# Kernel tuning notes

Measured on AMD Instinct MI355X. Metric: run time of the kernel, lower is better.

Reference implementation:

```python
import jax, jax.numpy as jnp
import numpy as np

N_NODES = 1_000_000
N_EDGES = 16_000_000
D = 30            # num_feature hardcoded in the module
WINDOW = D // 6   # = 5
DEG_THRESH = 10
NUM_TYPES = 2


def setup_inputs() -> dict:
    key = jax.random.key(0)
    k1, k2, k3, k4 = jax.random.split(key, 4)
    x = jax.random.normal(k1, (N_NODES, D), dtype=jnp.float32)
    W = jax.random.normal(k2, (D, D), dtype=jnp.float32)
    edge_index = jax.random.randint(k3, (2, N_EDGES), 0, N_NODES, dtype=jnp.int64)
    atom_types = jax.random.randint(k4, (N_NODES,), 0, NUM_TYPES, dtype=jnp.int64)
    return {"x": x, "W": W, "edge_index": edge_index, "atom_types": atom_types}


def reference(x, W, edge_index, atom_types):
    n = x.shape[0]
    # --- degree count: torch.bincount(edge_index.reshape(-1)) ---
    flat = edge_index.reshape(-1)
    count = jnp.zeros((n,), jnp.int32).at[flat].add(1)
    crit_count = (count > DEG_THRESH).astype(jnp.int32)  # criterion_count

    # --- type-mixture scatter-min over edges ---
    src, dst = edge_index[0], edge_index[1]
    same = atom_types[src] == atom_types[dst]
    # edge contributes 0 if types differ, else type+1, to BOTH endpoints; take min
    val = jnp.where(same, atom_types[src].astype(jnp.int32) + 1, 0)
    BIG = jnp.iinfo(jnp.int32).max
    mix = jnp.full((n,), BIG, jnp.int32)
    mix = mix.at[src].min(val).at[dst].min(val)
    mix = jnp.where(mix == BIG, 0, mix)  # isolated atoms -> 0

    crit = crit_count * 3 + mix  # criterion in [0, 5]

    # --- windowed one-hot criterion matrix [n, D] ---
    cols = jnp.arange(D, dtype=jnp.int32)
    start = (crit * WINDOW)[:, None]
    mask = ((cols[None, :] >= start) & (cols[None, :] < start + WINDOW)).astype(x.dtype)

    # --- e3nn Linear (30x0e -> 30x0e): dense matmul with 1/sqrt(fan_in) path norm ---
    scale = np.float32(1.0 / np.sqrt(D))
    return (x @ W) * scale * mask
```

## Files before the change

kernel.cpp:

```cpp
#include <hip/hip_runtime.h>

#define N_NODES    1000000
#define N_EDGES    16000000
#define D          30
#define WINDOW     5
#define DEG_THRESH 10

#define P_PARTS    31
#define PART_BITS  15
#define PART_SIZE  32768
#define CAP        1081344
#define BUF_CAP    512
#define BIN_BLOCKS 256
#define BIN_THREADS 1024
#define BIN_ITERS  16
#define N_GROUPS   (N_EDGES / 4)
#define BM_WORDS   (N_NODES / 32)

#define L_BM_BYTES   125000
#define L_BUF_BYTES  (P_PARTS * BUF_CAP * 2)
#define L_CNT_OFF    (L_BM_BYTES + L_BUF_BYTES)
#define L_TOTAL      (L_CNT_OFF + P_PARTS * 4 * 3)

#define SLICES     8
#define HIST_WORDS 16384

#define WS_BM_OFF      0
#define WS_CUR_OFF     131072
#define WS_PART_OFF    131328
#define WS_NEEDED      (WS_PART_OFF + (size_t)P_PARTS * SLICES * HIST_WORDS * 4)
#define OUT_BYTES_NEEDED ((size_t)P_PARTS * CAP * 2)

__global__ __launch_bounds__(256) void pack_types(
    const int* __restrict__ types,
    unsigned*  __restrict__ bm,
    unsigned*  __restrict__ cursors)
{
    const int g = blockIdx.x * 256 + threadIdx.x;
    const int v = (g < N_NODES) ? types[g] : 0;
    const unsigned long long m = __ballot(v);
    if ((threadIdx.x & 31) == 0 && g < N_NODES)
        bm[g >> 5] = (unsigned)(m >> (threadIdx.x & 32));
    if (blockIdx.x == 0 && threadIdx.x < 64) cursors[threadIdx.x] = 0u;
}

__global__ __launch_bounds__(BIN_THREADS, 1) void bin_edges(
    const int*      __restrict__ edge_index,
    const unsigned* __restrict__ bm,
    unsigned short* __restrict__ buckets,
    unsigned*       __restrict__ cursors)
{
    extern __shared__ char smem[];
    unsigned* bm_lds = (unsigned*)smem;
    unsigned short (*buf)[BUF_CAP] =
        (unsigned short(*)[BUF_CAP])(smem + L_BM_BYTES);
    unsigned* cnt   = (unsigned*)(smem + L_CNT_OFF);
    unsigned* basev = cnt + P_PARTS;
    unsigned* ccnt  = basev + P_PARTS;

    const int tid = threadIdx.x;
    for (int i = tid; i < BM_WORDS; i += BIN_THREADS) bm_lds[i] = bm[i];
    if (tid < P_PARTS) cnt[tid] = 0u;
    __syncthreads();

    for (int it = 0; it < BIN_ITERS; ++it) {
        const int g = (blockIdx.x * BIN_ITERS + it) * BIN_THREADS + tid;
        if (g < N_GROUPS) {
            const int e0 = g * 4;
            const int4 s4 = *reinterpret_cast<const int4*>(edge_index + e0);
            const int4 d4 = *reinterpret_cast<const int4*>(edge_index + N_EDGES + e0);
            const int ss[4] = {s4.x, s4.y, s4.z, s4.w};
            const int dd[4] = {d4.x, d4.y, d4.z, d4.w};
#pragma unroll
            for (int k = 0; k < 4; ++k) {
                const int s = ss[k], d = dd[k];
                const unsigned ts = (bm_lds[(unsigned)s >> 5] >> (s & 31)) & 1u;
                const unsigned td = (bm_lds[(unsigned)d >> 5] >> (d & 31)) & 1u;
                {
                    const int b = s >> PART_BITS;
                    const unsigned short rec =
                        (unsigned short)(((s & (PART_SIZE - 1)) << 1) | td);
                    const unsigned pos = atomicAdd(&cnt[b], 1u);
                    if (pos < BUF_CAP) buf[b][pos] = rec;
                    else {
                        const unsigned gp = atomicAdd(&cursors[b], 1u);
                        if (gp < CAP) buckets[(size_t)b * CAP + gp] = rec;
                    }
                }
                {
                    const int b = d >> PART_BITS;
                    const unsigned short rec =
                        (unsigned short)(((d & (PART_SIZE - 1)) << 1) | ts);
                    const unsigned pos = atomicAdd(&cnt[b], 1u);
                    if (pos < BUF_CAP) buf[b][pos] = rec;
                    else {
                        const unsigned gp = atomicAdd(&cursors[b], 1u);
                        if (gp < CAP) buckets[(size_t)b * CAP + gp] = rec;
                    }
                }
            }
        }
        __syncthreads();
        if (tid < P_PARTS) {
            unsigned c = cnt[tid]; if (c > BUF_CAP) c = BUF_CAP;
            unsigned bse = 0u;
            if (c) {
                bse = atomicAdd(&cursors[tid], c);
                if (bse > CAP) bse = CAP;
                if (bse + c > CAP) c = CAP - bse;
            }
            ccnt[tid] = c; basev[tid] = bse; cnt[tid] = 0u;
        }
        __syncthreads();
        const int w = tid >> 6, lane = tid & 63;
#pragma unroll
        for (int j = 0; j < 2; ++j) {
            const int b = w * 2 + j;
            if (b < P_PARTS) {
                const unsigned c = ccnt[b];
                unsigned short* dst = buckets + (size_t)b * CAP + basev[b];
                for (unsigned e = lane; e < c; e += 64) dst[e] = buf[b][e];
            }
        }
        __syncthreads();
    }
}

__global__ __launch_bounds__(512) void hist_pass(
    const unsigned short* __restrict__ buckets,
    const unsigned*       __restrict__ cursors,
    unsigned*             __restrict__ partials)
{
    __shared__ unsigned hist[HIST_WORDS];
    const int p = blockIdx.x >> 3, s = blockIdx.x & 7;
    const int tid = threadIdx.x;
    for (int i = tid; i < HIST_WORDS; i += 512) hist[i] = 0u;
    __syncthreads();

    unsigned count = cursors[p]; if (count > CAP) count = CAP;
    const unsigned short* bk = buckets + (size_t)p * CAP;
    const unsigned n4 = (count + 3u) >> 2;
    for (unsigned j = (unsigned)(s * 512 + tid); j < n4; j += SLICES * 512) {
        const unsigned i0 = j * 4u;
        if (i0 + 4u <= count) {
            const ushort4 r4 = *reinterpret_cast<const ushort4*>(bk + i0);
            const unsigned short rr[4] = {r4.x, r4.y, r4.z, r4.w};
#pragma unroll
            for (int k = 0; k < 4; ++k) {
                const unsigned rec = rr[k];
                const unsigned local = rec >> 1, t = rec & 1u;
                atomicAdd(&hist[local >> 1], (1u << (8u * t)) << (16u * (local & 1u)));
            }
        } else {
            for (unsigned i = i0; i < count; ++i) {
                const unsigned rec = bk[i];
                const unsigned local = rec >> 1, t = rec & 1u;
                atomicAdd(&hist[local >> 1], (1u << (8u * t)) << (16u * (local & 1u)));
            }
        }
    }
    __syncthreads();
    unsigned* op = partials + (size_t)blockIdx.x * HIST_WORDS;
    for (int i = tid; i < 512 * 32; i += 512) op[i] = hist[i];
}

#define WT_STRIDE  36
#define OT_THREADS 256
#define OT_ROWPAD  33
__global__ __launch_bounds__(OT_THREADS) void out_pass(
    const float* __restrict__ x, const float* __restrict__ Wm,
    const unsigned* __restrict__ partials,
    const unsigned* __restrict__ bm,
    float* __restrict__ out)
{
    __shared__ float sWt[D * WT_STRIDE];
    __shared__ float stg[OT_THREADS / 64][64 * OT_ROWPAD];
    const int tid = threadIdx.x;
    for (int i = tid; i < D * D; i += OT_THREADS) {
        const int k = i / D, c = i - k * D;
        sWt[c * WT_STRIDE + k] = Wm[i];
    }

    const int wv = tid >> 6, lane = tid & 63;
    const long blockBase = (long)blockIdx.x * OT_THREADS;
    const long waveBase  = blockBase + (long)wv * 64;
    float* ws = stg[wv];
    const long f2base = waveBase * 15;
    const long f2lim  = (long)N_NODES * 15;

    const float2* gx = reinterpret_cast<const float2*>(x);
#pragma unroll
    for (int it = 0; it < 15; ++it) {
        const int g = it * 64 + lane;
        const int row = g / 15, c2 = g - row * 15;
        float2 v = make_float2(0.0f, 0.0f);
        if (f2base + g < f2lim) v = gx[f2base + g];
        ws[row * OT_ROWPAD + 2 * c2]     = v.x;
        ws[row * OT_ROWPAD + 2 * c2 + 1] = v.y;
    }
    __syncthreads();

    const long n = blockBase + tid;
    int start = 0;
    if (n < N_NODES) {
        const unsigned Wd   = (unsigned)(n >> 1);
        const unsigned h    = (unsigned)n & 1u;
        const unsigned p    = Wd >> 14;
        const unsigned widx = Wd & 16383u;
        const unsigned* pp  = partials + (size_t)(p * SLICES) * HIST_WORDS + widx;
        unsigned sum = 0u;
#pragma unroll
        for (int s = 0; s < SLICES; ++s) sum += pp[(size_t)s * HIST_WORDS];
        const unsigned c0 = (sum >> (16u * h)) & 0xFFu;
        const unsigned c1 = (sum >> (16u * h + 8u)) & 0xFFu;
        const unsigned t  = (bm[n >> 5] >> ((unsigned)n & 31u)) & 1u;
        const unsigned cnt    = c0 + c1;
        const unsigned same_c = t ? c1 : c0;
        const unsigned diff_c = t ? c0 : c1;
        const int mix  = diff_c ? 0 : (same_c ? (int)t + 1 : 0);
        const int crit = (cnt > DEG_THRESH ? 3 : 0) + mix;
        start = crit * WINDOW;
    }

    float xr[D];
#pragma unroll
    for (int k = 0; k < D; ++k) xr[k] = ws[lane * OT_ROWPAD + k];

    float acc[WINDOW];
    const float* wc0 = &sWt[start * WT_STRIDE];
#pragma unroll
    for (int j = 0; j < WINDOW; ++j) {
        const float* wc = wc0 + j * WT_STRIDE;
        float a = 0.0f;
#pragma unroll
        for (int k = 0; k < D; ++k) a += xr[k] * wc[k];
        acc[j] = a * 0.18257418583505536f;
    }
    __syncthreads();

    float* wr = ws + lane * OT_ROWPAD;
#pragma unroll
    for (int k = 0; k < D; ++k) wr[k] = 0.0f;
#pragma unroll
    for (int j = 0; j < WINDOW; ++j) wr[start + j] = acc[j];
    __syncthreads();

    float2* gout = reinterpret_cast<float2*>(out);
#pragma unroll
    for (int it = 0; it < 15; ++it) {
        const int g = it * 64 + lane;
        const int row = g / 15, c2 = g - row * 15;
        if (f2base + g < f2lim)
            gout[f2base + g] = make_float2(ws[row * OT_ROWPAD + 2 * c2],
                                           ws[row * OT_ROWPAD + 2 * c2 + 1]);
    }
}

#define SAME_INC (1u << 12)
#define DIFF_INC (1u << 22)

__global__ __launch_bounds__(256) void edge_pass_atomic(
    const int* __restrict__ edge_index, const int* __restrict__ atom_types,
    unsigned* __restrict__ agg)
{
    const int t  = blockIdx.x * blockDim.x + threadIdx.x;
    const int e0 = t * 4;
    if (e0 >= N_EDGES) return;
    const int4 s4 = *reinterpret_cast<const int4*>(edge_index + e0);
    const int4 d4 = *reinterpret_cast<const int4*>(edge_index + N_EDGES + e0);
    const int ss[4] = {s4.x, s4.y, s4.z, s4.w};
    const int dd[4] = {d4.x, d4.y, d4.z, d4.w};
#pragma unroll
    for (int k = 0; k < 4; ++k) {
        const int s = ss[k], d = dd[k];
        const unsigned add = 1u + ((atom_types[s] == atom_types[d]) ? SAME_INC : DIFF_INC);
        atomicAdd(agg + s, add);
        atomicAdd(agg + d, add);
    }
}

__global__ __launch_bounds__(256) void out_pass_agg(
    const float* __restrict__ x, const float* __restrict__ Wm,
    const unsigned* __restrict__ agg, const int* __restrict__ atom_types,
    float* __restrict__ out)
{
    __shared__ float sx[64 * D];
    __shared__ float sW[D * D];
    __shared__ int   sstart[64];
    const int tid   = threadIdx.x;
    const long base = (long)blockIdx.x * 64;
    for (int i = tid; i < D * D; i += 256) sW[i] = Wm[i];
    const float* xb = x + base * D;
    for (int i = tid; i < 64 * D; i += 256) sx[i] = xb[i];
    if (tid < 64) {
        const long n = base + tid;
        const unsigned a = agg[n];
        const int cnt = a & 0xFFFu, sc = (a >> 12) & 0x3FFu, dc = a >> 22;
        const int mix  = dc ? 0 : (sc ? atom_types[n] + 1 : 0);
        sstart[tid] = ((cnt > DEG_THRESH ? 3 : 0) + mix) * WINDOW;
    }
    __syncthreads();
    const float scale = 0.18257418583505536f;
    float* ob = out + base * D;
    for (int i = tid; i < 64 * D; i += 256) {
        const int nd = i / D, c = i - nd * D;
        float v = 0.0f;
        if ((unsigned)(c - sstart[nd]) < WINDOW) {
            float acc = 0.0f;
#pragma unroll
            for (int k = 0; k < D; ++k) acc += sx[nd * D + k] * sW[k * D + c];
            v = acc * scale;
        }
        ob[i] = v;
    }
}

extern "C" void kernel_launch(void* const* d_in, const int* in_sizes, int n_in,
                              void* d_out, int out_size, void* d_ws, size_t ws_size,
                              hipStream_t stream)
{
    const float* x          = (const float*)d_in[0];
    const float* Wm         = (const float*)d_in[1];
    const int*   edge_index = (const int*)d_in[2];
    const int*   atom_types = (const int*)d_in[3];
    float* out = (float*)d_out;

    if (ws_size >= WS_NEEDED && (size_t)out_size * 4 >= OUT_BYTES_NEEDED) {
        char* ws = (char*)d_ws;
        unsigned*       bm       = (unsigned*)(ws + WS_BM_OFF);
        unsigned*       cursors  = (unsigned*)(ws + WS_CUR_OFF);
        unsigned*       partials = (unsigned*)(ws + WS_PART_OFF);
        unsigned short* buckets  = (unsigned short*)d_out;

        pack_types<<<(N_NODES + 255) / 256, 256, 0, stream>>>(atom_types, bm, cursors);
        bin_edges<<<BIN_BLOCKS, BIN_THREADS, L_TOTAL, stream>>>(edge_index, bm,
                                                                buckets, cursors);
        hist_pass<<<P_PARTS * SLICES, 512, 0, stream>>>(buckets, cursors, partials);
        out_pass<<<(N_NODES + OT_THREADS - 1) / OT_THREADS, OT_THREADS, 0, stream>>>(
            x, Wm, partials, bm, out);
    } else {
        unsigned* agg = (unsigned*)d_ws;
        hipMemsetAsync(agg, 0x00, N_NODES * sizeof(unsigned), stream);
        edge_pass_atomic<<<(N_EDGES / 4) / 256, 256, 0, stream>>>(edge_index, atom_types, agg);
        out_pass_agg<<<N_NODES / 64, 256, 0, stream>>>(x, Wm, agg, atom_types, out);
    }
}
```

Baseline: 384.1 us.

## Prefetch next edge group, flush LDS buckets every two iterations with 32-bit stores

The edge-binning kernel now loads the next iteration's edge indices into registers while the current group is being processed. The shared-memory bucket buffers are enlarged so they are flushed to global memory only every second iteration instead of every iteration. Each flush lets one wave reserve its own partitions' space and broadcast the bases by shuffle, dropping one block barrier, and copies records as 32-bit words. The cost is more LDS and registers, and heavier per-flush overflow, so more records may spill through the slow global-atomic path.

```diff
diff --git a/kernel.cpp b/kernel.cpp
--- a/kernel.cpp
+++ b/kernel.cpp
@@ -10,7 +10,8 @@
 #define PART_BITS  15
 #define PART_SIZE  32768
 #define CAP        1081344
-#define BUF_CAP    512
+#define BUF_CAP    616
+#define FLUSH_EVERY 2
 #define BIN_BLOCKS 256
 #define BIN_THREADS 1024
 #define BIN_ITERS  16
@@ -20,7 +21,7 @@
 #define L_BM_BYTES   125000
 #define L_BUF_BYTES  (P_PARTS * BUF_CAP * 2)
 #define L_CNT_OFF    (L_BM_BYTES + L_BUF_BYTES)
-#define L_TOTAL      (L_CNT_OFF + P_PARTS * 4 * 3)
+#define L_TOTAL      (L_CNT_OFF + P_PARTS * 4)
 
 #define SLICES     8
 #define HIST_WORDS 16384
@@ -54,23 +55,36 @@
     unsigned* bm_lds = (unsigned*)smem;
     unsigned short (*buf)[BUF_CAP] =
         (unsigned short(*)[BUF_CAP])(smem + L_BM_BYTES);
-    unsigned* cnt   = (unsigned*)(smem + L_CNT_OFF);
-    unsigned* basev = cnt + P_PARTS;
-    unsigned* ccnt  = basev + P_PARTS;
-
-    const int tid = threadIdx.x;
+    unsigned* cnt = (unsigned*)(smem + L_CNT_OFF);
+
+    const int tid  = threadIdx.x;
+    const int w    = tid >> 6, lane = tid & 63;
     for (int i = tid; i < BM_WORDS; i += BIN_THREADS) bm_lds[i] = bm[i];
     if (tid < P_PARTS) cnt[tid] = 0u;
     __syncthreads();
 
+    const int gstart = blockIdx.x * (BIN_ITERS * BIN_THREADS) + tid;
+
+    int4 cs = make_int4(0, 0, 0, 0), cd = make_int4(0, 0, 0, 0);
+    if (gstart < N_GROUPS) {
+        const int e0 = gstart * 4;
+        cs = *reinterpret_cast<const int4*>(edge_index + e0);
+        cd = *reinterpret_cast<const int4*>(edge_index + N_EDGES + e0);
+    }
+
     for (int it = 0; it < BIN_ITERS; ++it) {
-        const int g = (blockIdx.x * BIN_ITERS + it) * BIN_THREADS + tid;
+        const int g  = gstart + it * BIN_THREADS;
+        const int gn = g + BIN_THREADS;
+        int4 ns = cs, nd = cd;
+        const bool nv = (it + 1 < BIN_ITERS) && (gn < N_GROUPS);
+        if (nv) {
+            const int e0 = gn * 4;
+            ns = *reinterpret_cast<const int4*>(edge_index + e0);
+            nd = *reinterpret_cast<const int4*>(edge_index + N_EDGES + e0);
+        }
         if (g < N_GROUPS) {
-            const int e0 = g * 4;
-            const int4 s4 = *reinterpret_cast<const int4*>(edge_index + e0);
-            const int4 d4 = *reinterpret_cast<const int4*>(edge_index + N_EDGES + e0);
-            const int ss[4] = {s4.x, s4.y, s4.z, s4.w};
-            const int dd[4] = {d4.x, d4.y, d4.z, d4.w};
+            const int ss[4] = {cs.x, cs.y, cs.z, cs.w};
+            const int dd[4] = {cd.x, cd.y, cd.z, cd.w};
 #pragma unroll
             for (int k = 0; k < 4; ++k) {
                 const int s = ss[k], d = dd[k];
@@ -100,29 +114,54 @@
                 }
             }
         }
-        __syncthreads();
-        if (tid < P_PARTS) {
-            unsigned c = cnt[tid]; if (c > BUF_CAP) c = BUF_CAP;
-            unsigned bse = 0u;
-            if (c) {
-                bse = atomicAdd(&cursors[tid], c);
-                if (bse > CAP) bse = CAP;
-                if (bse + c > CAP) c = CAP - bse;
-            }
-            ccnt[tid] = c; basev[tid] = bse; cnt[tid] = 0u;
-        }
-        __syncthreads();
-        const int w = tid >> 6, lane = tid & 63;
-#pragma unroll
-        for (int j = 0; j < 2; ++j) {
-            const int b = w * 2 + j;
-            if (b < P_PARTS) {
-                const unsigned c = ccnt[b];
-                unsigned short* dst = buckets + (size_t)b * CAP + basev[b];
-                for (unsigned e = lane; e < c; e += 64) dst[e] = buf[b][e];
-            }
-        }
-        __syncthreads();
+        cs = ns; cd = nd;
+
+        if ((it & (FLUSH_EVERY - 1)) == (FLUSH_EVERY - 1)) {
+            __syncthreads();
+            unsigned myc = 0u, mybase = 0u;
+            const int ab = w * 2 + lane;
+            if (lane < 2 && ab < P_PARTS) {
+                unsigned c = cnt[ab]; if (c > BUF_CAP) c = BUF_CAP;
+                unsigned bse = 0u;
+                if (c) {
+                    bse = atomicAdd(&cursors[ab], c);
+                    if (bse > CAP) bse = CAP;
+                    if (bse + c > CAP) c = CAP - bse;
+                }
+                cnt[ab] = 0u;
+                myc = c; mybase = bse;
+            }
+            const unsigned c0 = __shfl(myc, 0), base0 = __shfl(mybase, 0);
+            const unsigned c1 = __shfl(myc, 1), base1 = __shfl(mybase, 1);
+#pragma unroll
+            for (int j = 0; j < 2; ++j) {
+                const int b = w * 2 + j;
+                const unsigned c    = j ? c1 : c0;
+                const unsigned base = j ? base1 : base0;
+                if (b < P_PARTS && c > 0u) {
+                    unsigned short* dst = buckets + (size_t)b * CAP;
+                    const unsigned head = base & 1u;
+                    if (head && lane == 0) dst[base] = buf[b][0];
+                    const unsigned body = c - head;
+                    const unsigned n2   = body >> 1;
+                    unsigned* dst32 = reinterpret_cast<unsigned*>(dst + base + head);
+                    if (head == 0u) {
+                        const unsigned* src32 =
+                            reinterpret_cast<const unsigned*>(&buf[b][0]);
+                        for (unsigned e = lane; e < n2; e += 64)
+                            dst32[e] = src32[e];
+                    } else {
+                        for (unsigned e = lane; e < n2; e += 64) {
+                            const unsigned lo = buf[b][1 + 2 * e];
+                            const unsigned hi = buf[b][2 + 2 * e];
+                            dst32[e] = lo | (hi << 16);
+                        }
+                    }
+                    if ((body & 1u) && lane == 0) dst[base + c - 1] = buf[b][c - 1];
+                }
+            }
+            __syncthreads();
+        }
     }
 }
 
@@ -161,7 +200,7 @@
     }
     __syncthreads();
     unsigned* op = partials + (size_t)blockIdx.x * HIST_WORDS;
-    for (int i = tid; i < 512 * 32; i += 512) op[i] = hist[i];
+    for (int i = tid; i < HIST_WORDS; i += 512) op[i] = hist[i];
 }
 
 #define WT_STRIDE  36
```

New measurement: 518.4 us. +35.0%, slower.
